# Performance work log

Measured on AMD Instinct MI355X. Metric: run time of the kernel, lower is better.

## Reference

```python
import jax, jax.numpy as jnp
import numpy as np

B, T, H, K = 128, 4096, 128, 5


def logistic_logcdf(x, mean, log_scale):
    z = (x - mean) * jnp.exp(-log_scale)
    return jax.nn.log_sigmoid(z)


def logistic_logpdf(x, mean, log_scale):
    z = (x - mean) * jnp.exp(-log_scale)
    zh = z / 2
    return -2 * jnp.logaddexp(zh, -zh) - log_scale


def mixlogistic_logcdf(x, prior_logits, means, log_scales):
    x = x[..., None]
    log_pi = jax.nn.log_softmax(prior_logits, axis=-1)
    return jax.nn.logsumexp(log_pi + logistic_logcdf(x, means, log_scales), axis=-1)


def mixlogistic_logpdf(x, prior_logits, means, log_scales):
    x = x[..., None]
    log_pi = jax.nn.log_softmax(prior_logits, axis=-1)
    return jax.nn.logsumexp(log_pi + logistic_logpdf(x, means, log_scales), axis=-1)


def coupling_function(x, pi, mu, log_s):
    log_cdf = jnp.minimum(mixlogistic_logcdf(x, pi, mu, log_s), -1e-12)
    log_1m = jnp.log(-jnp.expm1(log_cdf))
    val = log_cdf - log_1m
    log_jac = mixlogistic_logpdf(x, pi, mu, log_s) - log_cdf - log_1m
    return val, log_jac


def gru_step(h, x, Wi, Wh, bi, bhn):
    # flax GRUCell: input denses have bias, hidden denses no bias except hn.
    gi = x @ Wi + bi                      # [B, 3H]
    gh = h @ Wh                           # [B, 3H]
    ir, iz, inn = jnp.split(gi, 3, axis=-1)
    hr, hz, hn = jnp.split(gh, 3, axis=-1)
    r = jax.nn.sigmoid(ir + hr)
    z = jax.nn.sigmoid(iz + hz)
    n = jnp.tanh(inn + r * (hn + bhn))
    return (1.0 - z) * n + z * h


def setup_inputs() -> dict:
    key = jax.random.key(0)
    ks = jax.random.split(key, 14)
    g = lambda i, shape: (jax.random.normal(ks[i], shape) * 0.08).astype(jnp.float32)
    return {
        's': jax.random.normal(ks[0], (B, T), jnp.float32),
        'x': jax.random.normal(ks[1], (B, T), jnp.float32),
        'eps': jax.random.logistic(ks[2], (B, T), jnp.float32),
        # encoder GRU (in_features=1)
        'Wi_e': g(3, (1, 3 * H)), 'Wh_e': g(4, (H, 3 * H)),
        'bi_e': jnp.zeros(3 * H, jnp.float32), 'bhn_e': jnp.zeros(H, jnp.float32),
        # decoder GRU (in_features=1+H)
        'Wi_d': g(5, (1 + H, 3 * H)), 'Wh_d': g(6, (H, 3 * H)),
        'bi_d': jnp.zeros(3 * H, jnp.float32), 'bhn_d': jnp.zeros(H, jnp.float32),
        # heads
        'W_shift': g(7, (H, 1)), 'b_shift': jnp.zeros(1, jnp.float32),
        'W_lsc': g(8, (H, 1)), 'b_lsc': jnp.zeros(1, jnp.float32),
        'W_pi': g(9, (H, K)), 'b_pi': jnp.zeros(K, jnp.float32),
        'W_mu': g(10, (H, K)), 'b_mu': jnp.zeros(K, jnp.float32),
        'W_ls': g(11, (H, K)), 'b_ls': jnp.zeros(K, jnp.float32),
    }


def reference(s, x, eps, Wi_e, Wh_e, bi_e, bhn_e, Wi_d, Wh_d, bi_d, bhn_d,
              W_shift, b_shift, W_lsc, b_lsc, W_pi, b_pi, W_mu, b_mu, W_ls, b_ls):
    Bn, Tn = s.shape
    Hn = Wh_e.shape[0]
    s3 = s[..., None]  # [B,T,1]
    x3 = x[..., None]

    # --- encoder: reverse GRU, outputs kept in scan (reversed) order ---
    def enc_step(h, xt):
        h = gru_step(h, xt, Wi_e, Wh_e, bi_e, bhn_e)
        return h, h

    x_rev = jnp.flip(x3, axis=1).transpose(1, 0, 2)  # [T,B,1]
    _, h_x = jax.lax.scan(enc_step, jnp.zeros((Bn, Hn), s.dtype), x_rev)
    h_x = h_x.transpose(1, 0, 2)  # [B,T,H]

    sc = jnp.concatenate([s3, h_x], axis=-1)  # [B,T,1+H]

    def dec_step(carry, xs_t):
        h, pred = carry
        inp, e = xs_t              # inp [B,1+H], e [B]
        inp = inp.at[:, 0].set(pred)
        h = gru_step(h, inp, Wi_d, Wh_d, bi_d, bhn_d)
        y = h
        shift = (y @ W_shift + b_shift)[:, 0]
        log_scale = (y @ W_lsc + b_lsc)[:, 0]
        pi = y @ W_pi + b_pi
        mu = y @ W_mu + b_mu
        log_s = y @ W_ls + b_ls
        val, log_jac = coupling_function(e, pi, mu, log_s)
        prediction = shift + val * jnp.exp(log_scale)
        # standard logistic logpdf(e) = -e - 2*softplus(-e)
        logp = (-e - 2 * jax.nn.softplus(-e)) - log_scale - log_jac
        return (h, prediction), (logp, prediction)

    carry0 = (jnp.zeros((Bn, Hn), s.dtype), jnp.zeros(Bn, s.dtype))
    xs = (sc.transpose(1, 0, 2), eps.T)
    _, (logp, preds) = jax.lax.scan(dec_step, carry0, xs)
    return logp.T, preds.T  # each [B,T]
```

## Files before the change

### kernel.cpp

```cpp
#include <hip/hip_runtime.h>
#include <hip/hip_fp16.h>

#define Tn 4096
#define Bn 128
#define Hn 128
#define G3 384
#define NTH 448

typedef unsigned short u16;
typedef unsigned int u32;
typedef _Float16 f16;
typedef _Float16 h2 __attribute__((ext_vector_type(2)));

__device__ __forceinline__ float sigm(float v) { return 1.f / (1.f + __expf(-v)); }
__device__ __forceinline__ float tanh_fast(float v) {
  v = fminf(fmaxf(v, -15.f), 15.f);
  float e = __expf(-2.f * v);
  return (1.f - e) / (1.f + e);
}
__device__ __forceinline__ u16 f2h(float f) { return __half_as_ushort(__float2half(f)); }
__device__ __forceinline__ float h2f(u16 u) { return __half2float(__ushort_as_half(u)); }
__device__ __forceinline__ h2 bch2(u32 v) { union { u32 u; h2 h; } t; t.u = v; return t.h; }
__device__ __forceinline__ u32 bcu32(h2 v) { union { u32 u; h2 h; } t; t.h = v; return t.u; }
__device__ __forceinline__ float fdot2f(h2 a, h2 b, float c) {
  return __builtin_amdgcn_fdot2(a, b, c, false);
}

__global__ __launch_bounds__(NTH, 1) void combo_kernel(
    const float* __restrict__ x, const float* __restrict__ Wi_e,
    const float* __restrict__ Wh_e, const float* __restrict__ bi_e,
    const float* __restrict__ bhn_e, u16* __restrict__ hx,
    float* __restrict__ enc_h,
    const float* __restrict__ eps, const float* __restrict__ Wi_d,
    const float* __restrict__ Wh_d, const float* __restrict__ bhn_d,
    const float* __restrict__ W_shift, const float* __restrict__ b_shift,
    const float* __restrict__ W_lsc, const float* __restrict__ b_lsc,
    const float* __restrict__ W_pi, const float* __restrict__ b_pi,
    const float* __restrict__ W_mu, const float* __restrict__ b_mu,
    const float* __restrict__ W_ls, const float* __restrict__ b_ls,
    const u16* __restrict__ gi2, float* __restrict__ out,
    float* __restrict__ dec_h, float* __restrict__ dec_pred,
    int enc_t0, int dec_t0, int Tc)
{
  const int j = threadIdx.x;
  __shared__ __align__(16) f16 Xp[Hn];
  __shared__ __align__(16) float g2[512];
  __shared__ __align__(16) u32 hwlp[17 * 68];
  __shared__ float hbias_l[20];
  __shared__ float pred_s;
  const int bid = blockIdx.x;
  const int jj = (j < 384) ? j : 0;

  if (bid < Bn) {
    if (enc_t0 < 0) return;
    const int b = bid, t0 = enc_t0;
    h2 wp[64];
#pragma unroll
    for (int k = 0; k < 64; ++k) {
      h2 t; t.x = (f16)Wh_e[(2 * k) * G3 + jj]; t.y = (f16)Wh_e[(2 * k + 1) * G3 + jj];
      wp[k] = t;
    }
    float wie = 0.f, bie = 0.f, bhn = 0.f, hm = 0.f;
    if (j < 384) { wie = Wi_e[j]; bie = bi_e[j]; }
    if (j < Hn) {
      bhn = bhn_e[j];
      hm = (t0 == 0) ? 0.f : enc_h[(long)b * Hn + j];
      Xp[j] = (f16)hm;
    }
    const float* xrow = x + (long)b * Tn;
    u16* hxrow2 = hx + ((long)b * Hn + (j < Hn ? j : 0)) * Tc;
    float xc0, xc1, xc2, xc3, xc4, xc5, xc6, xc7;
    {
      int base = Tn - 8 - t0; if (base < 0) base = 0;
      float4 v0 = *(const float4*)(xrow + base), v1 = *(const float4*)(xrow + base + 4);
      xc0 = v1.w; xc1 = v1.z; xc2 = v1.y; xc3 = v1.x;
      xc4 = v0.w; xc5 = v0.z; xc6 = v0.y; xc7 = v0.x;
    }
    __syncthreads();
    for (int i8 = 0; i8 < Tc; i8 += 8) {
      int nbase = Tn - 8 - t0 - (i8 + 8); if (nbase < 0) nbase = 0;
      float4 nv0 = *(const float4*)(xrow + nbase);
      float4 nv1 = *(const float4*)(xrow + nbase + 4);
      u32 hb0_ = 0, hb1_ = 0, hb2_ = 0, hb3_ = 0;
#pragma unroll
      for (int u = 0; u < 8; ++u) {
        const float xt = (u == 0) ? xc0 : (u == 1) ? xc1 : (u == 2) ? xc2
                        : (u == 3) ? xc3 : (u == 4) ? xc4 : (u == 5) ? xc5
                        : (u == 6) ? xc6 : xc7;
        if (j < 384) {
          const uint4* hp = (const uint4*)Xp;
          float a0 = 0.f, a1 = 0.f, a2 = 0.f, a3 = 0.f;
#pragma unroll
          for (int q = 0; q < 16; ++q) {
            uint4 hv = hp[q];
            a0 = fdot2f(bch2(hv.x), wp[4 * q + 0], a0);
            a1 = fdot2f(bch2(hv.y), wp[4 * q + 1], a1);
            a2 = fdot2f(bch2(hv.z), wp[4 * q + 2], a2);
            a3 = fdot2f(bch2(hv.w), wp[4 * q + 3], a3);
          }
          float gh = (a0 + a1) + (a2 + a3);
          float gi = fmaf(xt, wie, bie);
          if (j < 256) g2[j] = gh + gi;
          else { g2[j] = gh; g2[j + 128] = gi; }
        }
        __syncthreads();
        if (j < Hn) {
          float r = sigm(g2[j]);
          float z = sigm(g2[128 + j]);
          float n = tanh_fast(g2[384 + j] + r * (g2[256 + j] + bhn));
          float hn2 = (1.f - z) * n + z * hm;
          hm = hn2;
          Xp[j] = (f16)hn2;
          u16 hv = f2h(hn2);
          if (u == 0) hb0_ = hv; else if (u == 1) hb0_ |= ((u32)hv << 16);
          else if (u == 2) hb1_ = hv; else if (u == 3) hb1_ |= ((u32)hv << 16);
          else if (u == 4) hb2_ = hv; else if (u == 5) hb2_ |= ((u32)hv << 16);
          else if (u == 6) hb3_ = hv; else hb3_ |= ((u32)hv << 16);
        }
        __syncthreads();
      }
      if (j < Hn) {
        uint4 o; o.x = hb0_; o.y = hb1_; o.z = hb2_; o.w = hb3_;
        *(uint4*)(hxrow2 + i8) = o;
      }
      xc0 = nv1.w; xc1 = nv1.z; xc2 = nv1.y; xc3 = nv1.x;
      xc4 = nv0.w; xc5 = nv0.z; xc6 = nv0.y; xc7 = nv0.x;
    }
    if (j < Hn) enc_h[(long)b * Hn + j] = hm;
  } else {
    if (dec_t0 < 0) return;
    const int b = bid - Bn, t0 = dec_t0;
    h2 wp[64];
#pragma unroll
    for (int k = 0; k < 64; ++k) {
      h2 t; t.x = (f16)Wh_d[(2 * k) * G3 + jj]; t.y = (f16)Wh_d[(2 * k + 1) * G3 + jj];
      wp[k] = t;
    }
    float bhn = 0.f, wr0 = 0.f, wz0 = 0.f, wn0 = 0.f, hm = 0.f;
    if (j < Hn) {
      bhn = bhn_d[j];
      wr0 = Wi_d[j];
      wz0 = Wi_d[128 + j];
      wn0 = Wi_d[256 + j];
      hm = (t0 == 0) ? 0.f : dec_h[(long)b * Hn + j];
      Xp[j] = (f16)hm;
    }
    for (int idx = j; idx < 17 * 64; idx += NTH) {
      int o = idx >> 6, k2 = idx & 63;
      int ka = 2 * k2, kb = 2 * k2 + 1;
      float wa, wb;
      if (o == 0) { wa = W_shift[ka]; wb = W_shift[kb]; }
      else if (o == 1) { wa = W_lsc[ka]; wb = W_lsc[kb]; }
      else if (o < 7) { wa = W_pi[ka * 5 + o - 2]; wb = W_pi[kb * 5 + o - 2]; }
      else if (o < 12) { wa = W_mu[ka * 5 + o - 7]; wb = W_mu[kb * 5 + o - 7]; }
      else { wa = W_ls[ka * 5 + o - 12]; wb = W_ls[kb * 5 + o - 12]; }
      h2 t; t.x = (f16)wa; t.y = (f16)wb;
      hwlp[o * 68 + k2] = bcu32(t);
    }
    if (j < 17)
      hbias_l[j] = (j == 0) ? b_shift[0] : (j == 1) ? b_lsc[0] : (j < 7) ? b_pi[j - 2]
                 : (j < 12) ? b_mu[j - 7] : b_ls[j - 12];
    float predreg = (t0 == 0) ? 0.f : dec_pred[b];
    if (j == 384) pred_s = predreg;
    const u16* girow2 = gi2 + ((long)b * G3 + jj) * Tc;
    const float* erow = eps + (long)b * Tn;
    uint4 gA4 = {0, 0, 0, 0};
    float ep = 0.f, ec0 = 0, ec1 = 0, ec2 = 0, ec3 = 0, ec4 = 0, ec5 = 0, ec6 = 0, ec7 = 0;
    if (j < 384) {
      gA4 = *(const uint4*)(girow2);
    } else {
      float4 v0 = *(const float4*)(erow + t0), v1 = *(const float4*)(erow + t0 + 4);
      ec0 = v0.x; ec1 = v0.y; ec2 = v0.z; ec3 = v0.w;
      ec4 = v1.x; ec5 = v1.y; ec6 = v1.z; ec7 = v1.w;
    }
    float lp0 = 0, lp1 = 0, lp2 = 0, lp3 = 0, lp4 = 0, lp5 = 0, lp6 = 0, lp7 = 0;
    float pr0 = 0, pr1 = 0, pr2 = 0, pr3 = 0, pr4 = 0, pr5 = 0, pr6 = 0, pr7 = 0;
    __syncthreads();
    const int lane = j - 384;
    const int ho = lane >> 1, hs = lane & 1;
    float* outlp = out + (long)b * Tn + t0;
    float* outpr = out + (long)Bn * Tn + (long)b * Tn + t0;

    auto couple = [&](float e) -> float2 {
      float p = 0.f;
      if (lane < 34) {
        const uint4* hp4 = (const uint4*)Xp;
        const uint4* wr4 = (const uint4*)&hwlp[ho * 68 + hs * 32];
#pragma unroll
        for (int q = 0; q < 8; ++q) {
          uint4 hv = hp4[hs * 8 + q];
          uint4 wv = wr4[q];
          p = fdot2f(bch2(hv.x), bch2(wv.x), p);
          p = fdot2f(bch2(hv.y), bch2(wv.y), p);
          p = fdot2f(bch2(hv.z), bch2(wv.z), p);
          p = fdot2f(bch2(hv.w), bch2(wv.w), p);
        }
      }
      p += __shfl_xor(p, 1);
      float pb = p + hbias_l[lane < 34 ? ho : 0];
      const int lj2 = lane & 7;
      float pi_ = __shfl(pb, 4 + 2 * lj2);
      float mu_ = __shfl(pb, 14 + 2 * lj2);
      float ls_ = __shfl(pb, 24 + 2 * lj2);
      float shiftv = __shfl(pb, 0);
      float lscv = __shfl(pb, 2);
      const bool valid = (lane < 5);
      float wexp = valid ? __expf(pi_) : 0.f;
      float zz = (e - mu_) * __expf(-ls_);
      float uq = __expf(-fabsf(zz));
      float dq = 1.f / (1.f + uq);
      float sigp = (zz >= 0.f) ? dq : uq * dq;
      float sigq = (zz >= 0.f) ? uq * dq : dq;
      float pdfl = uq * dq * dq * __expf(-ls_);
      float c = wexp * sigp, m = wexp * sigq, pq = wexp * pdfl, S = wexp;
      c += __shfl_xor(c, 1, 8); m += __shfl_xor(m, 1, 8);
      pq += __shfl_xor(pq, 1, 8); S += __shfl_xor(S, 1, 8);
      c += __shfl_xor(c, 2, 8); m += __shfl_xor(m, 2, 8);
      pq += __shfl_xor(pq, 2, 8); S += __shfl_xor(S, 2, 8);
      c += __shfl_xor(c, 4, 8); m += __shfl_xor(m, 4, 8);
      pq += __shfl_xor(pq, 4, 8); S += __shfl_xor(S, 4, 8);
      float logc = __logf(c), logm = __logf(m);
      float val = logc - logm;
      float ljac = __logf(pq) + __logf(S) - logc - logm;
      float prednew = fmaf(val, __expf(lscv), shiftv);
      float sp = fmaxf(-e, 0.f) + log1pf(__expf(-fabsf(e)));
      float logp = (-e - 2.f * sp) - lscv - ljac;
      return make_float2(logp, prednew);
    };

    for (int i8 = 0; i8 < Tc; i8 += 8) {
      uint4 gB4 = {0, 0, 0, 0};
      float4 en0 = {0, 0, 0, 0}, en1 = {0, 0, 0, 0};
      if (j < 384) {
        int gn = i8 + 8; if (gn > Tc - 8) gn = Tc - 8;
        gB4 = *(const uint4*)(girow2 + gn);
      } else {
        int sn = t0 + i8 + 8; if (sn > Tn - 8) sn = Tn - 8;
        en0 = *(const float4*)(erow + sn);
        en1 = *(const float4*)(erow + sn + 4);
      }
#pragma unroll
      for (int u = 0; u < 8; ++u) {
        const int i = i8 + u;
        if (j < 384) {
          const uint4* hp = (const uint4*)Xp;
          float a0 = 0.f, a1 = 0.f, a2 = 0.f, a3 = 0.f;
#pragma unroll
          for (int q = 0; q < 16; ++q) {
            uint4 hv = hp[q];
            a0 = fdot2f(bch2(hv.x), wp[4 * q + 0], a0);
            a1 = fdot2f(bch2(hv.y), wp[4 * q + 1], a1);
            a2 = fdot2f(bch2(hv.z), wp[4 * q + 2], a2);
            a3 = fdot2f(bch2(hv.w), wp[4 * q + 3], a3);
          }
          float gh = (a0 + a1) + (a2 + a3);
          u16 gv = (u == 0) ? (u16)gA4.x : (u == 1) ? (u16)(gA4.x >> 16)
                 : (u == 2) ? (u16)gA4.y : (u == 3) ? (u16)(gA4.y >> 16)
                 : (u == 4) ? (u16)gA4.z : (u == 5) ? (u16)(gA4.z >> 16)
                 : (u == 6) ? (u16)gA4.w : (u16)(gA4.w >> 16);
          float gipre = h2f(gv);
          if (j < 256) g2[j] = gh + gipre;
          else { g2[j] = gh; g2[j + 128] = gipre; }
        } else if (i >= 1) {
          float e = (u == 0) ? ep : (u == 1) ? ec0 : (u == 2) ? ec1 : (u == 3) ? ec2
                  : (u == 4) ? ec3 : (u == 5) ? ec4 : (u == 6) ? ec5 : ec6;
          float2 rr = couple(e);
          if (lane == 0) {
            if (u == 0) { lp7 = rr.x; pr7 = rr.y; }
            else if (u == 1) { lp0 = rr.x; pr0 = rr.y; }
            else if (u == 2) { lp1 = rr.x; pr1 = rr.y; }
            else if (u == 3) { lp2 = rr.x; pr2 = rr.y; }
            else if (u == 4) { lp3 = rr.x; pr3 = rr.y; }
            else if (u == 5) { lp4 = rr.x; pr4 = rr.y; }
            else if (u == 6) { lp5 = rr.x; pr5 = rr.y; }
            else { lp6 = rr.x; pr6 = rr.y; }
            pred_s = rr.y;
            predreg = rr.y;
            if (u == 0 && i8 > 0) {
              *(float4*)(outlp + i8 - 8) = make_float4(lp0, lp1, lp2, lp3);
              *(float4*)(outlp + i8 - 4) = make_float4(lp4, lp5, lp6, lp7);
              *(float4*)(outpr + i8 - 8) = make_float4(pr0, pr1, pr2, pr3);
              *(float4*)(outpr + i8 - 4) = make_float4(pr4, pr5, pr6, pr7);
            }
          }
        }
        __syncthreads();
        if (j < Hn) {
          float pred = pred_s;
          float r = sigm(fmaf(pred, wr0, g2[j]));
          float z = sigm(fmaf(pred, wz0, g2[128 + j]));
          float n = tanh_fast(fmaf(pred, wn0, g2[384 + j]) + r * (g2[256 + j] + bhn));
          float hn2 = (1.f - z) * n + z * hm;
          hm = hn2;
          Xp[j] = (f16)hn2;
        }
        __syncthreads();
      }
      gA4 = gB4;
      if (j >= 384) {
        ep = ec7;
        ec0 = en0.x; ec1 = en0.y; ec2 = en0.z; ec3 = en0.w;
        ec4 = en1.x; ec5 = en1.y; ec6 = en1.z; ec7 = en1.w;
      }
    }
    if (j >= 384) {
      float2 rr = couple(ep);
      if (lane == 0) {
        lp7 = rr.x; pr7 = rr.y; predreg = rr.y;
        *(float4*)(outlp + Tc - 8) = make_float4(lp0, lp1, lp2, lp3);
        *(float4*)(outlp + Tc - 4) = make_float4(lp4, lp5, lp6, lp7);
        *(float4*)(outpr + Tc - 8) = make_float4(pr0, pr1, pr2, pr3);
        *(float4*)(outpr + Tc - 4) = make_float4(pr4, pr5, pr6, pr7);
      }
    }
    if (j < Hn) dec_h[(long)b * Hn + j] = hm;
    if (j == 384) dec_pred[b] = predreg;
  }
}

__global__ __launch_bounds__(256) void gemm_gi(
    const u16* __restrict__ A2, const float* __restrict__ Wi_d,
    const float* __restrict__ bi_d, u16* __restrict__ C2, int Tc)
{
  __shared__ __align__(16) float As[16][64];
  __shared__ __align__(16) float Ws[16][64];
  const int tid = threadIdx.x;
  const long m0 = (long)blockIdx.x * 64;
  const int n0 = blockIdx.y * 64;
  const int bb = (int)(m0 / Tc);
  const int tt0 = (int)(m0 - (long)bb * Tc);
  const int tx = tid & 15, ty = tid >> 4;
  const int lk = tid >> 4, lm = (tid & 15) * 4;
  const int wk = tid >> 4, wn = (tid & 15) * 4;
  float acc[4][4] = {};
  for (int k0 = 0; k0 < Hn; k0 += 16) {
    uint2 a2v = *(const uint2*)(A2 + ((long)bb * Hn + k0 + lk) * Tc + tt0 + lm);
    float4 w4 = *(const float4*)(Wi_d + (long)(1 + k0 + wk) * G3 + n0 + wn);
    __syncthreads();
    As[lk][lm + 0] = h2f((u16)(a2v.x & 0xffffu));
    As[lk][lm + 1] = h2f((u16)(a2v.x >> 16));
    As[lk][lm + 2] = h2f((u16)(a2v.y & 0xffffu));
    As[lk][lm + 3] = h2f((u16)(a2v.y >> 16));
    *(float4*)&Ws[wk][wn] = w4;
    __syncthreads();
#pragma unroll
    for (int kk = 0; kk < 16; ++kk) {
      float4 av = *(const float4*)&As[kk][ty * 4];
      float4 wv = *(const float4*)&Ws[kk][tx * 4];
      float ar[4] = {av.x, av.y, av.z, av.w};
      float wr[4] = {wv.x, wv.y, wv.z, wv.w};
#pragma unroll
      for (int i = 0; i < 4; ++i)
#pragma unroll
        for (int jj = 0; jj < 4; ++jj) acc[i][jj] = fmaf(ar[i], wr[jj], acc[i][jj]);
    }
  }
  const float4 bbv = *(const float4*)(bi_d + n0 + tx * 4);
  const float br[4] = {bbv.x, bbv.y, bbv.z, bbv.w};
#pragma unroll
  for (int jj = 0; jj < 4; ++jj) {
    int colc = n0 + tx * 4 + jj;
    u32 lo = (u32)f2h(acc[0][jj] + br[jj]) | ((u32)f2h(acc[1][jj] + br[jj]) << 16);
    u32 hi = (u32)f2h(acc[2][jj] + br[jj]) | ((u32)f2h(acc[3][jj] + br[jj]) << 16);
    uint2 o; o.x = lo; o.y = hi;
    *(uint2*)(C2 + ((long)bb * G3 + colc) * Tc + tt0 + ty * 4) = o;
  }
}

extern "C" void kernel_launch(void* const* d_in, const int* in_sizes, int n_in,
                              void* d_out, int out_size, void* d_ws, size_t ws_size,
                              hipStream_t stream) {
  const float* x = (const float*)d_in[1];
  const float* eps = (const float*)d_in[2];
  const float* Wi_e = (const float*)d_in[3];
  const float* Wh_e = (const float*)d_in[4];
  const float* bi_e = (const float*)d_in[5];
  const float* bhn_e = (const float*)d_in[6];
  const float* Wi_d = (const float*)d_in[7];
  const float* Wh_d = (const float*)d_in[8];
  const float* bi_d = (const float*)d_in[9];
  const float* bhn_d = (const float*)d_in[10];
  const float* W_shift = (const float*)d_in[11];
  const float* b_shift = (const float*)d_in[12];
  const float* W_lsc = (const float*)d_in[13];
  const float* b_lsc = (const float*)d_in[14];
  const float* W_pi = (const float*)d_in[15];
  const float* b_pi = (const float*)d_in[16];
  const float* W_mu = (const float*)d_in[17];
  const float* b_mu = (const float*)d_in[18];
  const float* W_ls = (const float*)d_in[19];
  const float* b_ls = (const float*)d_in[20];
  float* out = (float*)d_out;

  const size_t stateB = (size_t)(2 * Bn * Hn + Bn) * sizeof(float);
  const size_t stateAl = (stateB + 255) & ~(size_t)255;
  int Tc = 512;
  while (Tc > 64 && stateAl + (size_t)Bn * Tc * (Hn + G3) * 2 > ws_size) Tc >>= 1;
  if (stateAl + (size_t)Bn * Tc * (Hn + G3) * 2 > ws_size) return;

  float* enc_h = (float*)d_ws;
  float* dec_h = enc_h + (size_t)Bn * Hn;
  float* dec_pred = dec_h + (size_t)Bn * Hn;
  u16* hx = (u16*)((char*)d_ws + stateAl);
  u16* gi = hx + (size_t)Bn * Tc * Hn;

  const int Nc = Tn / Tc;
  const dim3 gg((unsigned)(((size_t)Bn * Tc) / 64), G3 / 64);
  for (int k = 0; k <= Nc; ++k) {
    int enc_t0 = (k < Nc) ? k * Tc : -1;
    int dec_t0 = (k >= 1) ? (k - 1) * Tc : -1;
    combo_kernel<<<2 * Bn, NTH, 0, stream>>>(
        x, Wi_e, Wh_e, bi_e, bhn_e, hx, enc_h,
        eps, Wi_d, Wh_d, bhn_d, W_shift, b_shift, W_lsc, b_lsc,
        W_pi, b_pi, W_mu, b_mu, W_ls, b_ls,
        gi, out, dec_h, dec_pred, enc_t0, dec_t0, Tc);
    if (k < Nc) gemm_gi<<<gg, 256, 0, stream>>>(hx, Wi_d, bi_d, gi, Tc);
  }
}
```

Measured before the change: 5.793 ms.

## Fuse GRU gate matvec and update per thread, double-buffer hidden state

Cuts the block from 448 to 192 threads so each of 128 threads computes all three gate dot products (r, z, n) for its hidden unit and applies the gate nonlinearities directly. This removes the g2 shared-memory exchange and one barrier per encoder step. Xp is double-buffered so the next state can be written while the current one is still being read. Head weights move from shared memory into registers of the coupling warp, and the prefetch of gi/eps one chunk ahead is dropped. The trade-offs are three times the dot-product work per thread, much higher register pressure (192 h2 weight registers), and less latency hiding from the removed prefetch.

```diff
diff --git a/kernel.cpp b/kernel.cpp
--- a/kernel.cpp
+++ b/kernel.cpp
@@ -5,7 +5,7 @@
 #define Bn 128
 #define Hn 128
 #define G3 384
-#define NTH 448
+#define NTH 192
 
 typedef unsigned short u16;
 typedef unsigned int u32;
@@ -21,7 +21,6 @@
 __device__ __forceinline__ u16 f2h(float f) { return __half_as_ushort(__float2half(f)); }
 __device__ __forceinline__ float h2f(u16 u) { return __half2float(__ushort_as_half(u)); }
 __device__ __forceinline__ h2 bch2(u32 v) { union { u32 u; h2 h; } t; t.u = v; return t.h; }
-__device__ __forceinline__ u32 bcu32(h2 v) { union { u32 u; h2 h; } t; t.h = v; return t.u; }
 __device__ __forceinline__ float fdot2f(h2 a, h2 b, float c) {
   return __builtin_amdgcn_fdot2(a, b, c, false);
 }
@@ -43,161 +42,159 @@
     int enc_t0, int dec_t0, int Tc)
 {
   const int j = threadIdx.x;
-  __shared__ __align__(16) f16 Xp[Hn];
-  __shared__ __align__(16) float g2[512];
-  __shared__ __align__(16) u32 hwlp[17 * 68];
-  __shared__ float hbias_l[20];
+  __shared__ __align__(16) f16 Xp[2][Hn];
   __shared__ float pred_s;
   const int bid = blockIdx.x;
-  const int jj = (j < 384) ? j : 0;
+  int cur = 0;
 
   if (bid < Bn) {
     if (enc_t0 < 0) return;
     const int b = bid, t0 = enc_t0;
-    h2 wp[64];
-#pragma unroll
-    for (int k = 0; k < 64; ++k) {
-      h2 t; t.x = (f16)Wh_e[(2 * k) * G3 + jj]; t.y = (f16)Wh_e[(2 * k + 1) * G3 + jj];
-      wp[k] = t;
-    }
-    float wie = 0.f, bie = 0.f, bhn = 0.f, hm = 0.f;
-    if (j < 384) { wie = Wi_e[j]; bie = bi_e[j]; }
+    h2 wr_[64], wz_[64], wn_[64];
+    float wieR = 0, wieZ = 0, wieN = 0, bieR = 0, bieZ = 0, bieN = 0;
+    float bhn = 0, hm = 0;
     if (j < Hn) {
+#pragma unroll
+      for (int q = 0; q < 64; ++q) {
+        h2 a, bq, c;
+        a.x = (f16)Wh_e[(2 * q) * G3 + j];        a.y = (f16)Wh_e[(2 * q + 1) * G3 + j];
+        bq.x = (f16)Wh_e[(2 * q) * G3 + 128 + j]; bq.y = (f16)Wh_e[(2 * q + 1) * G3 + 128 + j];
+        c.x = (f16)Wh_e[(2 * q) * G3 + 256 + j];  c.y = (f16)Wh_e[(2 * q + 1) * G3 + 256 + j];
+        wr_[q] = a; wz_[q] = bq; wn_[q] = c;
+      }
+      wieR = Wi_e[j]; wieZ = Wi_e[128 + j]; wieN = Wi_e[256 + j];
+      bieR = bi_e[j]; bieZ = bi_e[128 + j]; bieN = bi_e[256 + j];
       bhn = bhn_e[j];
       hm = (t0 == 0) ? 0.f : enc_h[(long)b * Hn + j];
-      Xp[j] = (f16)hm;
-    }
+      Xp[0][j] = (f16)hm;
+    }
+    __syncthreads();
     const float* xrow = x + (long)b * Tn;
-    u16* hxrow2 = hx + ((long)b * Hn + (j < Hn ? j : 0)) * Tc;
-    float xc0, xc1, xc2, xc3, xc4, xc5, xc6, xc7;
-    {
-      int base = Tn - 8 - t0; if (base < 0) base = 0;
-      float4 v0 = *(const float4*)(xrow + base), v1 = *(const float4*)(xrow + base + 4);
-      xc0 = v1.w; xc1 = v1.z; xc2 = v1.y; xc3 = v1.x;
-      xc4 = v0.w; xc5 = v0.z; xc6 = v0.y; xc7 = v0.x;
-    }
-    __syncthreads();
+    u16* hxrow = hx + ((long)b * Hn + (j < Hn ? j : 0)) * Tc;
     for (int i8 = 0; i8 < Tc; i8 += 8) {
-      int nbase = Tn - 8 - t0 - (i8 + 8); if (nbase < 0) nbase = 0;
-      float4 nv0 = *(const float4*)(xrow + nbase);
-      float4 nv1 = *(const float4*)(xrow + nbase + 4);
-      u32 hb0_ = 0, hb1_ = 0, hb2_ = 0, hb3_ = 0;
+      float xc0 = 0, xc1 = 0, xc2 = 0, xc3 = 0, xc4 = 0, xc5 = 0, xc6 = 0, xc7 = 0;
+      u32 hb0 = 0, hb1 = 0, hb2 = 0, hb3 = 0;
+      if (j < Hn) {
+        int base = Tn - 8 - t0 - i8; if (base < 0) base = 0;
+        float4 v0 = *(const float4*)(xrow + base);
+        float4 v1 = *(const float4*)(xrow + base + 4);
+        xc0 = v1.w; xc1 = v1.z; xc2 = v1.y; xc3 = v1.x;
+        xc4 = v0.w; xc5 = v0.z; xc6 = v0.y; xc7 = v0.x;
+      }
 #pragma unroll
       for (int u = 0; u < 8; ++u) {
-        const float xt = (u == 0) ? xc0 : (u == 1) ? xc1 : (u == 2) ? xc2
-                        : (u == 3) ? xc3 : (u == 4) ? xc4 : (u == 5) ? xc5
-                        : (u == 6) ? xc6 : xc7;
-        if (j < 384) {
-          const uint4* hp = (const uint4*)Xp;
-          float a0 = 0.f, a1 = 0.f, a2 = 0.f, a3 = 0.f;
+        if (j < Hn) {
+          const uint4* hp = (const uint4*)Xp[cur];
+          float a0r = 0, a1r = 0, a0z = 0, a1z = 0, a0n = 0, a1n = 0;
 #pragma unroll
           for (int q = 0; q < 16; ++q) {
             uint4 hv = hp[q];
-            a0 = fdot2f(bch2(hv.x), wp[4 * q + 0], a0);
-            a1 = fdot2f(bch2(hv.y), wp[4 * q + 1], a1);
-            a2 = fdot2f(bch2(hv.z), wp[4 * q + 2], a2);
-            a3 = fdot2f(bch2(hv.w), wp[4 * q + 3], a3);
+            a0r = fdot2f(bch2(hv.x), wr_[4 * q + 0], a0r);
+            a1r = fdot2f(bch2(hv.y), wr_[4 * q + 1], a1r);
+            a0r = fdot2f(bch2(hv.z), wr_[4 * q + 2], a0r);
+            a1r = fdot2f(bch2(hv.w), wr_[4 * q + 3], a1r);
+            a0z = fdot2f(bch2(hv.x), wz_[4 * q + 0], a0z);
+            a1z = fdot2f(bch2(hv.y), wz_[4 * q + 1], a1z);
+            a0z = fdot2f(bch2(hv.z), wz_[4 * q + 2], a0z);
+            a1z = fdot2f(bch2(hv.w), wz_[4 * q + 3], a1z);
+            a0n = fdot2f(bch2(hv.x), wn_[4 * q + 0], a0n);
+            a1n = fdot2f(bch2(hv.y), wn_[4 * q + 1], a1n);
+            a0n = fdot2f(bch2(hv.z), wn_[4 * q + 2], a0n);
+            a1n = fdot2f(bch2(hv.w), wn_[4 * q + 3], a1n);
           }
-          float gh = (a0 + a1) + (a2 + a3);
-          float gi = fmaf(xt, wie, bie);
-          if (j < 256) g2[j] = gh + gi;
-          else { g2[j] = gh; g2[j + 128] = gi; }
+          const float xt = (u == 0) ? xc0 : (u == 1) ? xc1 : (u == 2) ? xc2
+                          : (u == 3) ? xc3 : (u == 4) ? xc4 : (u == 5) ? xc5
+                          : (u == 6) ? xc6 : xc7;
+          float r = sigm((a0r + a1r) + fmaf(xt, wieR, bieR));
+          float z = sigm((a0z + a1z) + fmaf(xt, wieZ, bieZ));
+          float n = tanh_fast(fmaf(xt, wieN, bieN) + r * ((a0n + a1n) + bhn));
+          hm = (1.f - z) * n + z * hm;
+          Xp[cur ^ 1][j] = (f16)hm;
+          u16 hv16 = f2h(hm);
+          if (u == 0) hb0 = hv16; else if (u == 1) hb0 |= ((u32)hv16 << 16);
+          else if (u == 2) hb1 = hv16; else if (u == 3) hb1 |= ((u32)hv16 << 16);
+          else if (u == 4) hb2 = hv16; else if (u == 5) hb2 |= ((u32)hv16 << 16);
+          else if (u == 6) hb3 = hv16; else hb3 |= ((u32)hv16 << 16);
         }
         __syncthreads();
-        if (j < Hn) {
-          float r = sigm(g2[j]);
-          float z = sigm(g2[128 + j]);
-          float n = tanh_fast(g2[384 + j] + r * (g2[256 + j] + bhn));
-          float hn2 = (1.f - z) * n + z * hm;
-          hm = hn2;
-          Xp[j] = (f16)hn2;
-          u16 hv = f2h(hn2);
-          if (u == 0) hb0_ = hv; else if (u == 1) hb0_ |= ((u32)hv << 16);
-          else if (u == 2) hb1_ = hv; else if (u == 3) hb1_ |= ((u32)hv << 16);
-          else if (u == 4) hb2_ = hv; else if (u == 5) hb2_ |= ((u32)hv << 16);
-          else if (u == 6) hb3_ = hv; else hb3_ |= ((u32)hv << 16);
-        }
-        __syncthreads();
+        cur ^= 1;
       }
       if (j < Hn) {
-        uint4 o; o.x = hb0_; o.y = hb1_; o.z = hb2_; o.w = hb3_;
-        *(uint4*)(hxrow2 + i8) = o;
-      }
-      xc0 = nv1.w; xc1 = nv1.z; xc2 = nv1.y; xc3 = nv1.x;
-      xc4 = nv0.w; xc5 = nv0.z; xc6 = nv0.y; xc7 = nv0.x;
+        uint4 o; o.x = hb0; o.y = hb1; o.z = hb2; o.w = hb3;
+        *(uint4*)(hxrow + i8) = o;
+      }
     }
     if (j < Hn) enc_h[(long)b * Hn + j] = hm;
   } else {
     if (dec_t0 < 0) return;
     const int b = bid - Bn, t0 = dec_t0;
-    h2 wp[64];
-#pragma unroll
-    for (int k = 0; k < 64; ++k) {
-      h2 t; t.x = (f16)Wh_d[(2 * k) * G3 + jj]; t.y = (f16)Wh_d[(2 * k + 1) * G3 + jj];
-      wp[k] = t;
-    }
-    float bhn = 0.f, wr0 = 0.f, wz0 = 0.f, wn0 = 0.f, hm = 0.f;
+    const int lane = j - 128;
+    h2 wr_[64], wz_[64], wn_[64];
+    h2 wp2[32];
+    float wr0 = 0, wz0 = 0, wn0 = 0, bhn = 0, hm = 0;
+    float hbias = 0, predreg = 0;
     if (j < Hn) {
+#pragma unroll
+      for (int q = 0; q < 64; ++q) {
+        h2 a, bq, c;
+        a.x = (f16)Wh_d[(2 * q) * G3 + j];        a.y = (f16)Wh_d[(2 * q + 1) * G3 + j];
+        bq.x = (f16)Wh_d[(2 * q) * G3 + 128 + j]; bq.y = (f16)Wh_d[(2 * q + 1) * G3 + 128 + j];
+        c.x = (f16)Wh_d[(2 * q) * G3 + 256 + j];  c.y = (f16)Wh_d[(2 * q + 1) * G3 + 256 + j];
+        wr_[q] = a; wz_[q] = bq; wn_[q] = c;
+      }
+      wr0 = Wi_d[j]; wz0 = Wi_d[128 + j]; wn0 = Wi_d[256 + j];
       bhn = bhn_d[j];
-      wr0 = Wi_d[j];
-      wz0 = Wi_d[128 + j];
-      wn0 = Wi_d[256 + j];
       hm = (t0 == 0) ? 0.f : dec_h[(long)b * Hn + j];
-      Xp[j] = (f16)hm;
-    }
-    for (int idx = j; idx < 17 * 64; idx += NTH) {
-      int o = idx >> 6, k2 = idx & 63;
-      int ka = 2 * k2, kb = 2 * k2 + 1;
-      float wa, wb;
-      if (o == 0) { wa = W_shift[ka]; wb = W_shift[kb]; }
-      else if (o == 1) { wa = W_lsc[ka]; wb = W_lsc[kb]; }
-      else if (o < 7) { wa = W_pi[ka * 5 + o - 2]; wb = W_pi[kb * 5 + o - 2]; }
-      else if (o < 12) { wa = W_mu[ka * 5 + o - 7]; wb = W_mu[kb * 5 + o - 7]; }
-      else { wa = W_ls[ka * 5 + o - 12]; wb = W_ls[kb * 5 + o - 12]; }
-      h2 t; t.x = (f16)wa; t.y = (f16)wb;
-      hwlp[o * 68 + k2] = bcu32(t);
-    }
-    if (j < 17)
-      hbias_l[j] = (j == 0) ? b_shift[0] : (j == 1) ? b_lsc[0] : (j < 7) ? b_pi[j - 2]
-                 : (j < 12) ? b_mu[j - 7] : b_ls[j - 12];
-    float predreg = (t0 == 0) ? 0.f : dec_pred[b];
-    if (j == 384) pred_s = predreg;
-    const u16* girow2 = gi2 + ((long)b * G3 + jj) * Tc;
+      Xp[0][j] = (f16)hm;
+    } else {
+      const int ho = lane >> 1, hs = lane & 1;
+      if (lane < 34) {
+#pragma unroll
+        for (int q = 0; q < 32; ++q) {
+          int ka = 2 * (hs * 32 + q), kb = ka + 1;
+          float wa, wb;
+          if (ho == 0) { wa = W_shift[ka]; wb = W_shift[kb]; }
+          else if (ho == 1) { wa = W_lsc[ka]; wb = W_lsc[kb]; }
+          else if (ho < 7) { wa = W_pi[ka * 5 + ho - 2]; wb = W_pi[kb * 5 + ho - 2]; }
+          else if (ho < 12) { wa = W_mu[ka * 5 + ho - 7]; wb = W_mu[kb * 5 + ho - 7]; }
+          else { wa = W_ls[ka * 5 + ho - 12]; wb = W_ls[kb * 5 + ho - 12]; }
+          h2 t; t.x = (f16)wa; t.y = (f16)wb;
+          wp2[q] = t;
+        }
+        hbias = (ho == 0) ? b_shift[0] : (ho == 1) ? b_lsc[0] : (ho < 7) ? b_pi[ho - 2]
+              : (ho < 12) ? b_mu[ho - 7] : b_ls[ho - 12];
+      } else {
+#pragma unroll
+        for (int q = 0; q < 32; ++q) { h2 t; t.x = (f16)0.f; t.y = (f16)0.f; wp2[q] = t; }
+      }
+      predreg = (t0 == 0) ? 0.f : dec_pred[b];
+      if (lane == 0) pred_s = predreg;
+    }
     const float* erow = eps + (long)b * Tn;
-    uint4 gA4 = {0, 0, 0, 0};
-    float ep = 0.f, ec0 = 0, ec1 = 0, ec2 = 0, ec3 = 0, ec4 = 0, ec5 = 0, ec6 = 0, ec7 = 0;
-    if (j < 384) {
-      gA4 = *(const uint4*)(girow2);
-    } else {
-      float4 v0 = *(const float4*)(erow + t0), v1 = *(const float4*)(erow + t0 + 4);
-      ec0 = v0.x; ec1 = v0.y; ec2 = v0.z; ec3 = v0.w;
-      ec4 = v1.x; ec5 = v1.y; ec6 = v1.z; ec7 = v1.w;
-    }
+    const u16* gibase = gi2 + (long)b * G3 * Tc;
+    float ep = 0.f;
     float lp0 = 0, lp1 = 0, lp2 = 0, lp3 = 0, lp4 = 0, lp5 = 0, lp6 = 0, lp7 = 0;
     float pr0 = 0, pr1 = 0, pr2 = 0, pr3 = 0, pr4 = 0, pr5 = 0, pr6 = 0, pr7 = 0;
-    __syncthreads();
-    const int lane = j - 384;
-    const int ho = lane >> 1, hs = lane & 1;
     float* outlp = out + (long)b * Tn + t0;
     float* outpr = out + (long)Bn * Tn + (long)b * Tn + t0;
-
-    auto couple = [&](float e) -> float2 {
+    __syncthreads();
+
+    auto couple = [&](float e, const f16* Xc) -> float2 {
+      const int hs = lane & 1;
       float p = 0.f;
       if (lane < 34) {
-        const uint4* hp4 = (const uint4*)Xp;
-        const uint4* wr4 = (const uint4*)&hwlp[ho * 68 + hs * 32];
+        const uint4* hp4 = (const uint4*)Xc;
 #pragma unroll
         for (int q = 0; q < 8; ++q) {
           uint4 hv = hp4[hs * 8 + q];
-          uint4 wv = wr4[q];
-          p = fdot2f(bch2(hv.x), bch2(wv.x), p);
-          p = fdot2f(bch2(hv.y), bch2(wv.y), p);
-          p = fdot2f(bch2(hv.z), bch2(wv.z), p);
-          p = fdot2f(bch2(hv.w), bch2(wv.w), p);
+          p = fdot2f(bch2(hv.x), wp2[4 * q + 0], p);
+          p = fdot2f(bch2(hv.y), wp2[4 * q + 1], p);
+          p = fdot2f(bch2(hv.z), wp2[4 * q + 2], p);
+          p = fdot2f(bch2(hv.w), wp2[4 * q + 3], p);
         }
       }
       p += __shfl_xor(p, 1);
-      float pb = p + hbias_l[lane < 34 ? ho : 0];
+      float pb = p + hbias;
       const int lj2 = lane & 7;
       float pi_ = __shfl(pb, 4 + 2 * lj2);
       float mu_ = __shfl(pb, 14 + 2 * lj2);
@@ -229,42 +226,46 @@
     };
 
     for (int i8 = 0; i8 < Tc; i8 += 8) {
-      uint4 gB4 = {0, 0, 0, 0};
-      float4 en0 = {0, 0, 0, 0}, en1 = {0, 0, 0, 0};
-      if (j < 384) {
-        int gn = i8 + 8; if (gn > Tc - 8) gn = Tc - 8;
-        gB4 = *(const uint4*)(girow2 + gn);
+      uint4 gR4 = {0, 0, 0, 0}, gZ4 = {0, 0, 0, 0}, gN4 = {0, 0, 0, 0};
+      float ec0 = 0, ec1 = 0, ec2 = 0, ec3 = 0, ec4 = 0, ec5 = 0, ec6 = 0, ec7 = 0;
+      if (j < Hn) {
+        gR4 = *(const uint4*)(gibase + (long)j * Tc + i8);
+        gZ4 = *(const uint4*)(gibase + (long)(128 + j) * Tc + i8);
+        gN4 = *(const uint4*)(gibase + (long)(256 + j) * Tc + i8);
       } else {
-        int sn = t0 + i8 + 8; if (sn > Tn - 8) sn = Tn - 8;
-        en0 = *(const float4*)(erow + sn);
-        en1 = *(const float4*)(erow + sn + 4);
+        float4 v0 = *(const float4*)(erow + t0 + i8);
+        float4 v1 = *(const float4*)(erow + t0 + i8 + 4);
+        ec0 = v0.x; ec1 = v0.y; ec2 = v0.z; ec3 = v0.w;
+        ec4 = v1.x; ec5 = v1.y; ec6 = v1.z; ec7 = v1.w;
       }
 #pragma unroll
       for (int u = 0; u < 8; ++u) {
         const int i = i8 + u;
-        if (j < 384) {
-          const uint4* hp = (const uint4*)Xp;
-          float a0 = 0.f, a1 = 0.f, a2 = 0.f, a3 = 0.f;
+        float ar = 0, az = 0, an = 0;
+        if (j < Hn) {
+          const uint4* hp = (const uint4*)Xp[cur];
+          float a0r = 0, a1r = 0, a0z = 0, a1z = 0, a0n = 0, a1n = 0;
 #pragma unroll
           for (int q = 0; q < 16; ++q) {
             uint4 hv = hp[q];
-            a0 = fdot2f(bch2(hv.x), wp[4 * q + 0], a0);
-            a1 = fdot2f(bch2(hv.y), wp[4 * q + 1], a1);
-            a2 = fdot2f(bch2(hv.z), wp[4 * q + 2], a2);
-            a3 = fdot2f(bch2(hv.w), wp[4 * q + 3], a3);
+            a0r = fdot2f(bch2(hv.x), wr_[4 * q + 0], a0r);
+            a1r = fdot2f(bch2(hv.y), wr_[4 * q + 1], a1r);
+            a0r = fdot2f(bch2(hv.z), wr_[4 * q + 2], a0r);
+            a1r = fdot2f(bch2(hv.w), wr_[4 * q + 3], a1r);
+            a0z = fdot2f(bch2(hv.x), wz_[4 * q + 0], a0z);
+            a1z = fdot2f(bch2(hv.y), wz_[4 * q + 1], a1z);
+            a0z = fdot2f(bch2(hv.z), wz_[4 * q + 2], a0z);
+            a1z = fdot2f(bch2(hv.w), wz_[4 * q + 3], a1z);
+            a0n = fdot2f(bch2(hv.x), wn_[4 * q + 0], a0n);
+            a1n = fdot2f(bch2(hv.y), wn_[4 * q + 1], a1n);
+            a0n = fdot2f(bch2(hv.z), wn_[4 * q + 2], a0n);
+            a1n = fdot2f(bch2(hv.w), wn_[4 * q + 3], a1n);
           }
-          float gh = (a0 + a1) + (a2 + a3);
-          u16 gv = (u == 0) ? (u16)gA4.x : (u == 1) ? (u16)(gA4.x >> 16)
-                 : (u == 2) ? (u16)gA4.y : (u == 3) ? (u16)(gA4.y >> 16)
-                 : (u == 4) ? (u16)gA4.z : (u == 5) ? (u16)(gA4.z >> 16)
-                 : (u == 6) ? (u16)gA4.w : (u16)(gA4.w >> 16);
-          float gipre = h2f(gv);
-          if (j < 256) g2[j] = gh + gipre;
-          else { g2[j] = gh; g2[j + 128] = gipre; }
+          ar = a0r + a1r; az = a0z + a1z; an = a0n + a1n;
         } else if (i >= 1) {
           float e = (u == 0) ? ep : (u == 1) ? ec0 : (u == 2) ? ec1 : (u == 3) ? ec2
                   : (u == 4) ? ec3 : (u == 5) ? ec4 : (u == 6) ? ec5 : ec6;
-          float2 rr = couple(e);
+          float2 rr = couple(e, Xp[cur]);
           if (lane == 0) {
             if (u == 0) { lp7 = rr.x; pr7 = rr.y; }
             else if (u == 1) { lp0 = rr.x; pr0 = rr.y; }
@@ -286,25 +287,32 @@
         }
         __syncthreads();
         if (j < Hn) {
+          u16 gvr = (u == 0) ? (u16)gR4.x : (u == 1) ? (u16)(gR4.x >> 16)
+                  : (u == 2) ? (u16)gR4.y : (u == 3) ? (u16)(gR4.y >> 16)
+                  : (u == 4) ? (u16)gR4.z : (u == 5) ? (u16)(gR4.z >> 16)
+                  : (u == 6) ? (u16)gR4.w : (u16)(gR4.w >> 16);
+          u16 gvz = (u == 0) ? (u16)gZ4.x : (u == 1) ? (u16)(gZ4.x >> 16)
+                  : (u == 2) ? (u16)gZ4.y : (u == 3) ? (u16)(gZ4.y >> 16)
+                  : (u == 4) ? (u16)gZ4.z : (u == 5) ? (u16)(gZ4.z >> 16)
+                  : (u == 6) ? (u16)gZ4.w : (u16)(gZ4.w >> 16);
+          u16 gvn = (u == 0) ? (u16)gN4.x : (u == 1) ? (u16)(gN4.x >> 16)
+                  : (u == 2) ? (u16)gN4.y : (u == 3) ? (u16)(gN4.y >> 16)
+                  : (u == 4) ? (u16)gN4.z : (u == 5) ? (u16)(gN4.z >> 16)
+                  : (u == 6) ? (u16)gN4.w : (u16)(gN4.w >> 16);
           float pred = pred_s;
-          float r = sigm(fmaf(pred, wr0, g2[j]));
-          float z = sigm(fmaf(pred, wz0, g2[128 + j]));
-          float n = tanh_fast(fmaf(pred, wn0, g2[384 + j]) + r * (g2[256 + j] + bhn));
-          float hn2 = (1.f - z) * n + z * hm;
-          hm = hn2;
-          Xp[j] = (f16)hn2;
+          float r = sigm(ar + h2f(gvr) + pred * wr0);
+          float z = sigm(az + h2f(gvz) + pred * wz0);
+          float n = tanh_fast(h2f(gvn) + pred * wn0 + r * (an + bhn));
+          hm = (1.f - z) * n + z * hm;
+          Xp[cur ^ 1][j] = (f16)hm;
         }
         __syncthreads();
-      }
-      gA4 = gB4;
-      if (j >= 384) {
-        ep = ec7;
-        ec0 = en0.x; ec1 = en0.y; ec2 = en0.z; ec3 = en0.w;
-        ec4 = en1.x; ec5 = en1.y; ec6 = en1.z; ec7 = en1.w;
-      }
-    }
-    if (j >= 384) {
-      float2 rr = couple(ep);
+        cur ^= 1;
+      }
+      if (j >= 128) ep = ec7;
+    }
+    if (j >= 128) {
+      float2 rr = couple(ep, Xp[cur]);
       if (lane == 0) {
         lp7 = rr.x; pr7 = rr.y; predreg = rr.y;
         *(float4*)(outlp + Tc - 8) = make_float4(lp0, lp1, lp2, lp3);
@@ -314,7 +322,7 @@
       }
     }
     if (j < Hn) dec_h[(long)b * Hn + j] = hm;
-    if (j == 384) dec_pred[b] = predreg;
+    if (j == 128) dec_pred[b] = predreg;
   }
 }
 
```

After: 5.693 ms. No clear change (-1.7%).
